# Performance work log

Measured on AMD Instinct MI355X. Metric: run time of the kernel, lower is better.

The kernel has to match this reference:

```python
import jax, jax.numpy as jnp
import numpy as np

N, C, G = 50000, 30, 1000   # cells, classes, genes
E = 800000                   # edges
OUT = 8                      # GATv2 out channels, heads=1


def setup_inputs() -> dict:
    key = jax.random.key(0)
    ks = jax.random.split(key, 12)
    X = jax.random.normal(ks[0], (N, G), dtype=jnp.float32)
    Mu = jax.random.normal(ks[1], (C, G), dtype=jnp.float32)
    Var = jax.random.uniform(ks[2], (C, G), dtype=jnp.float32) + 0.5  # strictly positive
    edge_index = jax.random.randint(ks[3], (2, E), 0, N, dtype=jnp.int64)
    # learned params
    W = 0.01 * jax.random.normal(ks[4], (N, C), dtype=jnp.float32)   # torch init zeros; small noise for nontrivial P
    S = jnp.ones((N, 1), dtype=jnp.float32)
    sc = 1.0 / np.sqrt(G)
    Wl = sc * jax.random.normal(ks[5], (OUT, G), dtype=jnp.float32)  # lin_l weight
    bl = jnp.zeros((OUT,), dtype=jnp.float32)
    Wr = sc * jax.random.normal(ks[6], (OUT, G), dtype=jnp.float32)  # lin_r weight
    br = jnp.zeros((OUT,), dtype=jnp.float32)
    att = jax.random.normal(ks[7], (OUT,), dtype=jnp.float32) / np.sqrt(OUT)
    return {"X": X, "Mu": Mu, "Var": Var, "edge_index": edge_index,
            "W": W, "S": S, "Wl": Wl, "bl": bl, "Wr": Wr, "br": br, "att": att}


def reference(X, Mu, Var, edge_index, W, S, Wl, bl, Wr, br, att):
    n = X.shape[0]
    P = jax.nn.softmax(W, axis=1)                       # [N,C]
    # Gaussian log-likelihood term. Expand (X - Mu*S)^2/Var summed over genes:
    invVar = 1.0 / Var                                  # [C,G]
    A = (X * X) @ invVar.T                              # [N,C]  sum X^2/Var
    B = X @ (Mu * invVar).T                             # [N,C]  sum X*Mu/Var
    D = jnp.sum(Mu * Mu * invVar, axis=1)               # [C]    sum Mu^2/Var
    Fmat = -0.5 * (A - 2.0 * S * B + (S * S) * D[None, :])  # [N,C]
    ll_prot = jnp.sum(P * Fmat) / n

    # GATv2 attention (heads=1, add_self_loops=False)
    x_l = X @ Wl.T + bl                                 # [N,8] source transform
    x_r = X @ Wr.T + br                                 # [N,8] target transform
    src, dst = edge_index[0], edge_index[1]
    m = jax.nn.leaky_relu(x_l[src] + x_r[dst], negative_slope=0.2)  # [E,8]
    e = m @ att                                         # [E]
    # edge-softmax grouped by destination node
    emax = jax.ops.segment_max(e, dst, num_segments=n)  # [N]
    e_exp = jnp.exp(e - emax[dst])                      # [E]
    denom = jax.ops.segment_sum(e_exp, dst, num_segments=n)  # [N]
    alpha = e_exp / (denom[dst] + 1e-16)                # [E]

    ce_space = -jnp.sum(P[src] * alpha[:, None] * jnp.log(P[dst] + 1e-8)) / n
    return ll_prot, ce_space, P
```

## Files before the change

### kernel.cpp

```cpp
#include <hip/hip_runtime.h>
#include <math.h>

#define N_CELLS 50000
#define C_CLS   30
#define G_GENES 1000
#define E_EDGES 800000
#define KPAD    1024
#define NREP    4

typedef __attribute__((ext_vector_type(8))) short bf16x8;
typedef __attribute__((ext_vector_type(4))) float f32x4;

__device__ __forceinline__ unsigned f2bf_u(float f) {
    unsigned u = __float_as_uint(f);
    return (u + 0x7fffu + ((u >> 16) & 1u)) >> 16;
}
__device__ __forceinline__ unsigned pack2(float lo, float hi) {
    return f2bf_u(lo) | (f2bf_u(hi) << 16);
}
__device__ __forceinline__ float bf2f(unsigned short u) {
    return __uint_as_float(((unsigned)u) << 16);
}

__device__ __forceinline__ float lrelu02(float v) { return v > 0.f ? v : 0.2f * v; }

__device__ __forceinline__ float dp4(int4 a, int4 b) {
    const unsigned* ua = (const unsigned*)&a;
    const unsigned* ub = (const unsigned*)&b;
    float s = 0.f;
#pragma unroll
    for (int i = 0; i < 4; i++) {
        float al = __uint_as_float(ua[i] << 16);
        float ah = __uint_as_float(ua[i] & 0xffff0000u);
        float bl = __uint_as_float(ub[i] << 16);
        float bh = __uint_as_float(ub[i] & 0xffff0000u);
        s += al * bl + ah * bh;
    }
    return s;
}

__global__ void prep_kernel(const float* __restrict__ Mu, const float* __restrict__ Var,
                            const float* __restrict__ Wl, const float* __restrict__ Wr,
                            unsigned short* __restrict__ CoefB, float* __restrict__ Dvec,
                            float* __restrict__ dn4, float* __restrict__ out) {
    const int r = blockIdx.x;
    const int t = threadIdx.x;
    __shared__ float red[256];
    float dacc = 0.f;
    for (int g = t; g < KPAD; g += 256) {
        float v = 0.f;
        if (g < G_GENES) {
            if (r < 30) {
                float iv = 1.0f / Var[r * G_GENES + g];
                float mu = Mu[r * G_GENES + g];
                v = iv;
                dacc += mu * mu * iv;
            } else if (r >= 32) {
                int i = r - 32;
                if (i < 30)      v = Mu[i * G_GENES + g] / Var[i * G_GENES + g];
                else if (i < 38) v = Wl[(i - 30) * G_GENES + g];
                else if (i < 46) v = Wr[(i - 38) * G_GENES + g];
            }
        }
        CoefB[r * KPAD + g] = (unsigned short)f2bf_u(v);
    }
    for (int i = blockIdx.x * 256 + t; i < N_CELLS * NREP * 2; i += 80 * 256) dn4[i] = 0.f;
    if (r == 31 && t < 2) out[t] = 0.f;

    if (r < 30) {
        red[t] = dacc;
        __syncthreads();
        for (int s = 128; s > 0; s >>= 1) {
            if (t < s) red[t] += red[t + s];
            __syncthreads();
        }
        if (t == 0) Dvec[r] = red[0];
    }
}

__global__ __launch_bounds__(256, 3) void main_rows_kernel(
    const float* __restrict__ X, const float* __restrict__ W,
    const float* __restrict__ S, const float* __restrict__ bl,
    const float* __restrict__ br, const unsigned short* __restrict__ CoefB,
    const float* __restrict__ Dvec,
    float* __restrict__ out,
    unsigned short* __restrict__ Pb, unsigned short* __restrict__ Lb,
    float* __restrict__ xl, float* __restrict__ xr)
{
    const int t    = threadIdx.x;
    const int w    = t >> 6;
    const int l    = t & 63;
    const int l15  = l & 15;
    const int quad = l >> 4;
    const int k0q  = quad * 8;
    const int wavebase = blockIdx.x * 64 + w * 16;
    if (wavebase >= N_CELLS) return;
    const float* __restrict__ xrow = X + (size_t)(wavebase + l15) * G_GENES;
    const unsigned short* __restrict__ cb = CoefB + (size_t)l15 * KPAD + k0q;

    f32x4 acc[5];
#pragma unroll
    for (int i = 0; i < 5; i++) acc[i] = (f32x4){0.f, 0.f, 0.f, 0.f};

    float4 c0a = *(const float4*)&xrow[k0q];
    float4 c0b = *(const float4*)&xrow[k0q + 4];
    float4 c1a = *(const float4*)&xrow[32 + k0q];
    float4 c1b = *(const float4*)&xrow[32 + k0q + 4];

#pragma unroll 2
    for (int kt = 0; kt < KPAD; kt += 64) {
        float4 n0a = make_float4(0.f, 0.f, 0.f, 0.f), n0b = n0a, n1a = n0a, n1b = n0a;
        const int ktn = kt + 64;
        if (ktn < KPAD) {
            const int ka = ktn + k0q;
            n0a = *(const float4*)&xrow[ka];
            n0b = *(const float4*)&xrow[ka + 4];
            const int kb = ktn + 32 + k0q;
            if (kb < G_GENES) {
                n1a = *(const float4*)&xrow[kb];
                n1b = *(const float4*)&xrow[kb + 4];
            }
        }

        union { unsigned u[4]; bf16x8 v; } ua, u2;
        ua.u[0] = pack2(c0a.x, c0a.y); ua.u[1] = pack2(c0a.z, c0a.w);
        ua.u[2] = pack2(c0b.x, c0b.y); ua.u[3] = pack2(c0b.z, c0b.w);
        u2.u[0] = pack2(c0a.x * c0a.x, c0a.y * c0a.y);
        u2.u[1] = pack2(c0a.z * c0a.z, c0a.w * c0a.w);
        u2.u[2] = pack2(c0b.x * c0b.x, c0b.y * c0b.y);
        u2.u[3] = pack2(c0b.z * c0b.z, c0b.w * c0b.w);
#pragma unroll
        for (int nt = 0; nt < 5; nt++) {
            bf16x8 b = *(const bf16x8*)&cb[(size_t)nt * 16 * KPAD + kt];
            acc[nt] = __builtin_amdgcn_mfma_f32_16x16x32_bf16(
                nt < 2 ? u2.v : ua.v, b, acc[nt], 0, 0, 0);
        }
        ua.u[0] = pack2(c1a.x, c1a.y); ua.u[1] = pack2(c1a.z, c1a.w);
        ua.u[2] = pack2(c1b.x, c1b.y); ua.u[3] = pack2(c1b.z, c1b.w);
        u2.u[0] = pack2(c1a.x * c1a.x, c1a.y * c1a.y);
        u2.u[1] = pack2(c1a.z * c1a.z, c1a.w * c1a.w);
        u2.u[2] = pack2(c1b.x * c1b.x, c1b.y * c1b.y);
        u2.u[3] = pack2(c1b.z * c1b.z, c1b.w * c1b.w);
#pragma unroll
        for (int nt = 0; nt < 5; nt++) {
            bf16x8 b = *(const bf16x8*)&cb[(size_t)nt * 16 * KPAD + kt + 32];
            acc[nt] = __builtin_amdgcn_mfma_f32_16x16x32_bf16(
                nt < 2 ? u2.v : ua.v, b, acc[nt], 0, 0, 0);
        }

        c0a = n0a; c0b = n0b; c1a = n1a; c1b = n1b;
    }

    const int rbase = wavebase + quad * 4;
    const bool c2ok = (l15 < 14);
    const float d0 = Dvec[l15];
    const float d1 = c2ok ? Dvec[16 + l15] : 0.f;
    float llacc = 0.f;
#pragma unroll
    for (int r = 0; r < 4; r++) {
        const int row = rbase + r;
        float w0 = W[(size_t)row * 30 + l15];
        float w1 = c2ok ? W[(size_t)row * 30 + 16 + l15] : -1e30f;
        float m = fmaxf(w0, w1);
#pragma unroll
        for (int mm = 1; mm < 16; mm <<= 1) m = fmaxf(m, __shfl_xor(m, mm, 64));
        float e0 = __expf(w0 - m);
        float e1 = c2ok ? __expf(w1 - m) : 0.f;
        float s = e0 + e1;
#pragma unroll
        for (int mm = 1; mm < 16; mm <<= 1) s += __shfl_xor(s, mm, 64);
        float inv = 1.0f / s;
        float p0 = e0 * inv, p1 = e1 * inv;
        float Sn = S[row], Sn2 = Sn * Sn;
        float F0 = -0.5f * (acc[0][r] - 2.0f * Sn * acc[2][r] + Sn2 * d0);
        float F1 = -0.5f * (acc[1][r] - 2.0f * Sn * acc[3][r] + Sn2 * d1);
        float lp = p0 * F0 + (c2ok ? p1 * F1 : 0.f);
#pragma unroll
        for (int mm = 1; mm < 16; mm <<= 1) lp += __shfl_xor(lp, mm, 64);
        llacc += lp;

        out[2 + (size_t)row * 30 + l15] = p0;
        float lg0 = __logf(p0 + 1e-8f);
        Pb[(size_t)row * 32 + l15] = (unsigned short)f2bf_u(p0);
        Lb[(size_t)row * 32 + l15] = (unsigned short)f2bf_u(lg0);
        if (c2ok) {
            out[2 + (size_t)row * 30 + 16 + l15] = p1;
            float lg1 = __logf(p1 + 1e-8f);
            Pb[(size_t)row * 32 + 16 + l15] = (unsigned short)f2bf_u(p1);
            Lb[(size_t)row * 32 + 16 + l15] = (unsigned short)f2bf_u(lg1);
        } else {
            Pb[(size_t)row * 32 + 16 + l15] = 0;
            Lb[(size_t)row * 32 + 16 + l15] = 0;
        }
        if (l15 >= 14)                xl[(size_t)row * 8 + (l15 - 14)] = acc[3][r] + bl[l15 - 14];
        else if (l15 < 6)             xl[(size_t)row * 8 + (l15 + 2)]  = acc[4][r] + bl[l15 + 2];
        if (l15 >= 6 && l15 < 14)     xr[(size_t)row * 8 + (l15 - 6)]  = acc[4][r] + br[l15 - 6];
    }
    llacc += __shfl_xor(llacc, 16, 64);
    llacc += __shfl_xor(llacc, 32, 64);
    if (l == 0) atomicAdd(&out[0], llacc * (1.0f / N_CELLS));
}

__global__ __launch_bounds__(256) void edge_pass(
    const int* __restrict__ ei, const float* __restrict__ xl,
    const float* __restrict__ xr, const float* __restrict__ att,
    const unsigned short* __restrict__ Pb, const unsigned short* __restrict__ Lb,
    float* __restrict__ dn4) {
    int e = blockIdx.x * 256 + threadIdx.x;
    if (e >= E_EDGES) return;
    int src = ei[e];
    int dst = ei[E_EDGES + e];
    const float4* lp = (const float4*)&xl[(size_t)src * 8];
    const float4* rp = (const float4*)&xr[(size_t)dst * 8];
    float4 l0 = lp[0], l1 = lp[1];
    float4 r0 = rp[0], r1 = rp[1];
    float ev = 0.f;
    ev += lrelu02(l0.x + r0.x) * att[0];
    ev += lrelu02(l0.y + r0.y) * att[1];
    ev += lrelu02(l0.z + r0.z) * att[2];
    ev += lrelu02(l0.w + r0.w) * att[3];
    ev += lrelu02(l1.x + r1.x) * att[4];
    ev += lrelu02(l1.y + r1.y) * att[5];
    ev += lrelu02(l1.z + r1.z) * att[6];
    ev += lrelu02(l1.w + r1.w) * att[7];
    float p = __expf(ev);

    const int4* ps = (const int4*)&Pb[(size_t)src * 32];
    const int4* ld = (const int4*)&Lb[(size_t)dst * 32];
    int4 a0 = ps[0], a1 = ps[1], a2 = ps[2], a3 = ps[3];
    int4 b0 = ld[0], b1 = ld[1], b2 = ld[2], b3 = ld[3];
    float dot = dp4(a0, b0) + dp4(a1, b1) + dp4(a2, b2) + dp4(a3, b3);

    float* base = &dn4[((size_t)(blockIdx.x & (NREP - 1)) * N_CELLS + dst) * 2];
    atomicAdd(base, p);
    atomicAdd(base + 1, p * dot);
}

__global__ __launch_bounds__(256) void finalize_kernel(const float* __restrict__ dn4,
                                                       float* __restrict__ out) {
    const int t = threadIdx.x;
    const int i = blockIdx.x * 256 + t;
    float c = 0.f;
    if (i < N_CELLS) {
        float d  = (dn4[(size_t)i * 2]     + dn4[((size_t)N_CELLS + i) * 2]) +
                   (dn4[((size_t)2 * N_CELLS + i) * 2] + dn4[((size_t)3 * N_CELLS + i) * 2]);
        float nm = (dn4[(size_t)i * 2 + 1] + dn4[((size_t)N_CELLS + i) * 2 + 1]) +
                   (dn4[((size_t)2 * N_CELLS + i) * 2 + 1] + dn4[((size_t)3 * N_CELLS + i) * 2 + 1]);
        c = nm / (d + 1e-16f);
    }
#pragma unroll
    for (int m = 1; m < 64; m <<= 1) c += __shfl_xor(c, m, 64);
    __shared__ float wsum[4];
    if ((t & 63) == 0) wsum[t >> 6] = c;
    __syncthreads();
    if (t == 0)
        atomicAdd(&out[1], -(wsum[0] + wsum[1] + wsum[2] + wsum[3]) * (1.0f / N_CELLS));
}

extern "C" void kernel_launch(void* const* d_in, const int* in_sizes, int n_in,
                              void* d_out, int out_size, void* d_ws, size_t ws_size,
                              hipStream_t stream) {
    const float* X   = (const float*)d_in[0];
    const float* Mu  = (const float*)d_in[1];
    const float* Var = (const float*)d_in[2];
    const int*   ei  = (const int*)d_in[3];
    const float* W   = (const float*)d_in[4];
    const float* S   = (const float*)d_in[5];
    const float* Wl  = (const float*)d_in[6];
    const float* bl  = (const float*)d_in[7];
    const float* Wr  = (const float*)d_in[8];
    const float* br  = (const float*)d_in[9];
    const float* att = (const float*)d_in[10];

    float* out = (float*)d_out;

    float* wsf = (float*)d_ws;
    unsigned short* CoefB  = (unsigned short*)wsf;
    float* Dvec            = wsf + 40960;
    unsigned short* Pb     = (unsigned short*)(wsf + 40992);
    unsigned short* Lb     = (unsigned short*)(wsf + 840992);
    float* xl              = wsf + 1640992;
    float* xr              = wsf + 2040992;
    float* dn4             = wsf + 2440992;

    prep_kernel<<<80, 256, 0, stream>>>(Mu, Var, Wl, Wr, CoefB, Dvec, dn4, out);
    main_rows_kernel<<<(N_CELLS + 63) / 64, 256, 0, stream>>>(
        X, W, S, bl, br, CoefB, Dvec, out, Pb, Lb, xl, xr);
    edge_pass<<<(E_EDGES + 255) / 256, 256, 0, stream>>>(ei, xl, xr, att, Pb, Lb, dn4);
    finalize_kernel<<<(N_CELLS + 255) / 256, 256, 0, stream>>>(dn4, out);
}
```

Baseline: 472.7 us.

## Stage coefficient tiles in LDS, split edges across lanes, use hardware bf16 pack

The main rows kernel now stages the CoefB coefficient tiles through double-buffered shared memory, where each block previously read them from global memory per wave. It also raises the occupancy hint to 4 blocks per SM. The edge pass now gives each edge four lanes that split the feature and class dot products and combine them with shuffles, aiming for coalesced gathers and more memory-level parallelism. The float-to-bf16 packing switches to the HIP intrinsic. Together these add barriers, LDS pressure and possible register spills under the tighter launch bound.

```diff
diff --git a/kernel.cpp b/kernel.cpp
--- a/kernel.cpp
+++ b/kernel.cpp
@@ -1,4 +1,5 @@
 #include <hip/hip_runtime.h>
+#include <hip/hip_bf16.h>
 #include <math.h>
 
 #define N_CELLS 50000
@@ -16,7 +17,9 @@
     return (u + 0x7fffu + ((u >> 16) & 1u)) >> 16;
 }
 __device__ __forceinline__ unsigned pack2(float lo, float hi) {
-    return f2bf_u(lo) | (f2bf_u(hi) << 16);
+    union { __hip_bfloat162 h; unsigned u; } cv;
+    cv.h = __float22bfloat162_rn(make_float2(lo, hi));
+    return cv.u;
 }
 __device__ __forceinline__ float bf2f(unsigned short u) {
     return __uint_as_float(((unsigned)u) << 16);
@@ -78,7 +81,7 @@
     }
 }
 
-__global__ __launch_bounds__(256, 3) void main_rows_kernel(
+__global__ __launch_bounds__(256, 4) void main_rows_kernel(
     const float* __restrict__ X, const float* __restrict__ W,
     const float* __restrict__ S, const float* __restrict__ bl,
     const float* __restrict__ br, const unsigned short* __restrict__ CoefB,
@@ -87,6 +90,8 @@
     unsigned short* __restrict__ Pb, unsigned short* __restrict__ Lb,
     float* __restrict__ xl, float* __restrict__ xr)
 {
+    __shared__ __align__(16) unsigned short Ct[2][80 * 72];
+
     const int t    = threadIdx.x;
     const int w    = t >> 6;
     const int l    = t & 63;
@@ -94,24 +99,52 @@
     const int quad = l >> 4;
     const int k0q  = quad * 8;
     const int wavebase = blockIdx.x * 64 + w * 16;
-    if (wavebase >= N_CELLS) return;
+    const bool valid = (wavebase < N_CELLS);
     const float* __restrict__ xrow = X + (size_t)(wavebase + l15) * G_GENES;
-    const unsigned short* __restrict__ cb = CoefB + (size_t)l15 * KPAD + k0q;
+
+    const int srow = t >> 3;
+    const int scol = (t & 7) << 3;
+    const bool s3  = (t < 128);
+    const unsigned short* __restrict__ cb0 = &CoefB[srow * KPAD + scol];
 
     f32x4 acc[5];
 #pragma unroll
     for (int i = 0; i < 5; i++) acc[i] = (f32x4){0.f, 0.f, 0.f, 0.f};
 
-    float4 c0a = *(const float4*)&xrow[k0q];
-    float4 c0b = *(const float4*)&xrow[k0q + 4];
-    float4 c1a = *(const float4*)&xrow[32 + k0q];
-    float4 c1b = *(const float4*)&xrow[32 + k0q + 4];
+    {
+        int4 p0 = *(const int4*)(cb0);
+        int4 p1 = *(const int4*)(cb0 + 32 * KPAD);
+        *(int4*)&Ct[0][srow * 72 + scol] = p0;
+        *(int4*)&Ct[0][(srow + 32) * 72 + scol] = p1;
+        if (s3) {
+            int4 p2 = *(const int4*)(cb0 + 64 * KPAD);
+            *(int4*)&Ct[0][(srow + 64) * 72 + scol] = p2;
+        }
+    }
+
+    float4 c0a = make_float4(0.f, 0.f, 0.f, 0.f), c0b = c0a, c1a = c0a, c1b = c0a;
+    if (valid) {
+        c0a = *(const float4*)&xrow[k0q];
+        c0b = *(const float4*)&xrow[k0q + 4];
+        c1a = *(const float4*)&xrow[32 + k0q];
+        c1b = *(const float4*)&xrow[32 + k0q + 4];
+    }
+    __syncthreads();
 
 #pragma unroll 2
     for (int kt = 0; kt < KPAD; kt += 64) {
+        const int cur = (kt >> 6) & 1;
+        const int ktn = kt + 64;
+
+        int4 q0, q1, q2;
+        if (ktn < KPAD) {
+            q0 = *(const int4*)(cb0 + ktn);
+            q1 = *(const int4*)(cb0 + 32 * KPAD + ktn);
+            if (s3) q2 = *(const int4*)(cb0 + 64 * KPAD + ktn);
+        }
+
         float4 n0a = make_float4(0.f, 0.f, 0.f, 0.f), n0b = n0a, n1a = n0a, n1b = n0a;
-        const int ktn = kt + 64;
-        if (ktn < KPAD) {
+        if (valid && ktn < KPAD) {
             const int ka = ktn + k0q;
             n0a = *(const float4*)&xrow[ka];
             n0b = *(const float4*)&xrow[ka + 4];
@@ -131,7 +164,7 @@
         u2.u[3] = pack2(c0b.z * c0b.z, c0b.w * c0b.w);
 #pragma unroll
         for (int nt = 0; nt < 5; nt++) {
-            bf16x8 b = *(const bf16x8*)&cb[(size_t)nt * 16 * KPAD + kt];
+            bf16x8 b = *(const bf16x8*)&Ct[cur][(nt * 16 + l15) * 72 + k0q];
             acc[nt] = __builtin_amdgcn_mfma_f32_16x16x32_bf16(
                 nt < 2 ? u2.v : ua.v, b, acc[nt], 0, 0, 0);
         }
@@ -143,13 +176,22 @@
         u2.u[3] = pack2(c1b.z * c1b.z, c1b.w * c1b.w);
 #pragma unroll
         for (int nt = 0; nt < 5; nt++) {
-            bf16x8 b = *(const bf16x8*)&cb[(size_t)nt * 16 * KPAD + kt + 32];
+            bf16x8 b = *(const bf16x8*)&Ct[cur][(nt * 16 + l15) * 72 + 32 + k0q];
             acc[nt] = __builtin_amdgcn_mfma_f32_16x16x32_bf16(
                 nt < 2 ? u2.v : ua.v, b, acc[nt], 0, 0, 0);
         }
 
+        if (ktn < KPAD) {
+            *(int4*)&Ct[cur ^ 1][srow * 72 + scol] = q0;
+            *(int4*)&Ct[cur ^ 1][(srow + 32) * 72 + scol] = q1;
+            if (s3) *(int4*)&Ct[cur ^ 1][(srow + 64) * 72 + scol] = q2;
+            __syncthreads();
+        }
+
         c0a = n0a; c0b = n0b; c1a = n1a; c1b = n1b;
     }
+
+    if (!valid) return;
 
     const int rbase = wavebase + quad * 4;
     const bool c2ok = (l15 < 14);
@@ -206,34 +248,30 @@
     const float* __restrict__ xr, const float* __restrict__ att,
     const unsigned short* __restrict__ Pb, const unsigned short* __restrict__ Lb,
     float* __restrict__ dn4) {
-    int e = blockIdx.x * 256 + threadIdx.x;
-    if (e >= E_EDGES) return;
-    int src = ei[e];
-    int dst = ei[E_EDGES + e];
-    const float4* lp = (const float4*)&xl[(size_t)src * 8];
-    const float4* rp = (const float4*)&xr[(size_t)dst * 8];
-    float4 l0 = lp[0], l1 = lp[1];
-    float4 r0 = rp[0], r1 = rp[1];
-    float ev = 0.f;
-    ev += lrelu02(l0.x + r0.x) * att[0];
-    ev += lrelu02(l0.y + r0.y) * att[1];
-    ev += lrelu02(l0.z + r0.z) * att[2];
-    ev += lrelu02(l0.w + r0.w) * att[3];
-    ev += lrelu02(l1.x + r1.x) * att[4];
-    ev += lrelu02(l1.y + r1.y) * att[5];
-    ev += lrelu02(l1.z + r1.z) * att[6];
-    ev += lrelu02(l1.w + r1.w) * att[7];
+    const int t = threadIdx.x;
+    const int g = t >> 2;
+    const int j = t & 3;
+    const int e = blockIdx.x * 64 + g;
+    const int src = ei[e];
+    const int dst = ei[E_EDGES + e];
+
+    float2 lv = *(const float2*)&xl[(size_t)src * 8 + j * 2];
+    float2 rv = *(const float2*)&xr[(size_t)dst * 8 + j * 2];
+    float2 av = *(const float2*)&att[j * 2];
+    float ev = lrelu02(lv.x + rv.x) * av.x + lrelu02(lv.y + rv.y) * av.y;
+    ev += __shfl_xor(ev, 1, 64);
+    ev += __shfl_xor(ev, 2, 64);
     float p = __expf(ev);
 
-    const int4* ps = (const int4*)&Pb[(size_t)src * 32];
-    const int4* ld = (const int4*)&Lb[(size_t)dst * 32];
-    int4 a0 = ps[0], a1 = ps[1], a2 = ps[2], a3 = ps[3];
-    int4 b0 = ld[0], b1 = ld[1], b2 = ld[2], b3 = ld[3];
-    float dot = dp4(a0, b0) + dp4(a1, b1) + dp4(a2, b2) + dp4(a3, b3);
+    int4 a = *(const int4*)&Pb[(size_t)src * 32 + j * 8];
+    int4 b = *(const int4*)&Lb[(size_t)dst * 32 + j * 8];
+    float dot = dp4(a, b);
+    dot += __shfl_xor(dot, 1, 64);
+    dot += __shfl_xor(dot, 2, 64);
 
     float* base = &dn4[((size_t)(blockIdx.x & (NREP - 1)) * N_CELLS + dst) * 2];
-    atomicAdd(base, p);
-    atomicAdd(base + 1, p * dot);
+    if (j == 0)      atomicAdd(base, p);
+    else if (j == 1) atomicAdd(base + 1, p * dot);
 }
 
 __global__ __launch_bounds__(256) void finalize_kernel(const float* __restrict__ dn4,
@@ -286,6 +324,6 @@
     prep_kernel<<<80, 256, 0, stream>>>(Mu, Var, Wl, Wr, CoefB, Dvec, dn4, out);
     main_rows_kernel<<<(N_CELLS + 63) / 64, 256, 0, stream>>>(
         X, W, S, bl, br, CoefB, Dvec, out, Pb, Lb, xl, xr);
-    edge_pass<<<(E_EDGES + 255) / 256, 256, 0, stream>>>(ei, xl, xr, att, Pb, Lb, dn4);
+    edge_pass<<<E_EDGES / 64, 256, 0, stream>>>(ei, xl, xr, att, Pb, Lb, dn4);
     finalize_kernel<<<(N_CELLS + 255) / 256, 256, 0, stream>>>(dn4, out);
 }
```

Result: faster. 443.6 us (-6.2%).
